# Kernel tuning notes

Hardware: AMD Instinct MI355X
Metric: run time of the kernel (lower is better)

The kernel has to match this reference:

```python
import jax, jax.numpy as jnp
import numpy as np
from jax import lax

B, N, S = 16, 8192, 512
BASE_K = 16
MS_K = (8, 16, 24)


def _fps(xyz, npoint):
    # farthest point sampling; xyz [B,N,3] -> indices [B,npoint]
    b, n, _ = xyz.shape
    def body(carry, _):
        dists, far = carry
        c = jnp.take_along_axis(xyz, far[:, None, None], axis=1)  # [B,1,3]
        d = jnp.sum((xyz - c) ** 2, -1)
        dists = jnp.minimum(dists, d)
        return (dists, jnp.argmax(dists, -1).astype(jnp.int32)), far
    init = (jnp.full((b, n), 1e10, xyz.dtype), jnp.zeros((b,), jnp.int32))
    _, idx = lax.scan(body, init, None, length=npoint)
    return idx.swapaxes(0, 1)  # [B,npoint]


def _sqdist(a, b):
    # a [B,S,3], b [B,N,3] -> squared distances [B,S,N] (same topk order as cdist)
    return (jnp.sum(a * a, -1)[:, :, None] + jnp.sum(b * b, -1)[:, None, :]
            - 2.0 * jnp.einsum('bsc,bnc->bsn', a, b))


def _gather(pts, idx):
    # pts [B,N,C], idx [B,S,K] -> [B,S,K,C]
    b = pts.shape[0]
    return pts[jnp.arange(b)[:, None, None], idx]


def setup_inputs():
    key = jax.random.key(0)
    ks = jax.random.split(key, 6)
    s = 0.05
    return {
        'l0_xyz': jax.random.normal(ks[0], (B, 3, N), jnp.float32),
        'l0_points': jax.random.normal(ks[1], (B, 3, N), jnp.float32),
        'sa_W1': jax.random.normal(ks[2], (64, 6), jnp.float32) * s,
        'sa_b1': jnp.zeros((64,), jnp.float32),
        'sa_W2': jax.random.normal(ks[3], (128, 64), jnp.float32) * s,
        'sa_b2': jnp.zeros((128,), jnp.float32),
        'ms_W1': jax.random.normal(ks[4], (3, 64, 3), jnp.float32) * s,
        'ms_b1': jnp.zeros((3, 64), jnp.float32),
        'ms_W2': jax.random.normal(ks[5], (3, 128, 64), jnp.float32) * s,
        'ms_b2': jnp.zeros((3, 128), jnp.float32),
    }


def reference(l0_xyz, l0_points, sa_W1, sa_b1, sa_W2, sa_b2, ms_W1, ms_b1, ms_W2, ms_b2):
    xyz = l0_xyz.swapaxes(1, 2)     # [B,N,3]
    pts = l0_points.swapaxes(1, 2)  # [B,N,3]
    # --- PointNet_SA_Module_KNN: FPS + KNN grouping + shared MLP + max-pool ---
    fps_idx = _fps(lax.stop_gradient(xyz), S)                         # [B,S]
    new_xyz = jnp.take_along_axis(xyz, fps_idx[:, :, None], axis=1)  # [B,S,3]
    d = _sqdist(lax.stop_gradient(new_xyz), lax.stop_gradient(xyz))  # [B,S,N]
    _, knn_idx = lax.top_k(-d, BASE_K)                                # [B,S,K]
    g_xyz = _gather(xyz, knn_idx) - new_xyz[:, :, None]               # [B,S,K,3]
    g_pts = _gather(pts, knn_idx)                                     # [B,S,K,3]
    feat = jnp.concatenate([g_xyz, g_pts], -1)                        # [B,S,K,6]
    h = jax.nn.relu(jnp.einsum('bskc,oc->bsko', feat, sa_W1) + sa_b1)
    h = jnp.einsum('bsko,po->bskp', h, sa_W2) + sa_b2
    base_feat = jnp.max(h, axis=2)                                    # [B,S,128]
    keypoints = new_xyz.swapaxes(1, 2)                                # [B,3,S]
    # --- multi-scale: no_grad cdist, per-scale topk + rel-coord MLP + max-pool ---
    dist = _sqdist(lax.stop_gradient(new_xyz), lax.stop_gradient(xyz))  # [B,S,N]
    feats = [base_feat.swapaxes(1, 2)]                                  # [B,128,S]
    for i, k in enumerate(MS_K):
        k_eff = min(k, N)
        _, idx = lax.top_k(-dist, k_eff)                                # [B,S,k]
        rel = _gather(xyz, idx) - new_xyz[:, :, None]                   # [B,S,k,3]
        h = jax.nn.relu(jnp.einsum('bskc,oc->bsko', rel, ms_W1[i]) + ms_b1[i])
        h = jnp.einsum('bsko,po->bskp', h, ms_W2[i]) + ms_b2[i]
        feats.append(jnp.max(h, axis=2).swapaxes(1, 2))                 # [B,128,S]
    return keypoints, jnp.concatenate(feats, axis=1)                    # [B,3,S],[B,512,S]
```

## Files before the change

kernel.cpp:

```cpp
#include <hip/hip_runtime.h>

#define BB 16
#define NN 8192
#define SS 512
#define N3 (3 * NN)
#define KD 14

typedef unsigned short u16;
typedef unsigned int u32;
typedef unsigned long long u64;
typedef float v2f __attribute__((ext_vector_type(2)));

__device__ __forceinline__ v2f pk_add(v2f a, v2f b) {
  v2f r;
  asm("v_pk_add_f32 %0, %1, %2" : "=v"(r) : "v"(a), "v"(b));
  return r;
}
__device__ __forceinline__ v2f pk_mul(v2f a, v2f b) {
  v2f r;
  asm("v_pk_mul_f32 %0, %1, %2" : "=v"(r) : "v"(a), "v"(b));
  return r;
}

template <int CTRL>
__device__ __forceinline__ u64 dpp_maxk(u64 k) {
  u32 lo = (u32)k, hi = (u32)(k >> 32);
  u32 slo = (u32)__builtin_amdgcn_update_dpp(0, (int)lo, CTRL, 0xf, 0xf, false);
  u32 shi = (u32)__builtin_amdgcn_update_dpp(0, (int)hi, CTRL, 0xf, 0xf, false);
  u64 s = ((u64)shi << 32) | (u64)slo;
  return (s > k) ? s : k;
}
__device__ __forceinline__ u64 maxk(u64 a, u64 b) { return (a > b) ? a : b; }

__global__ __attribute__((amdgpu_flat_work_group_size(512, 512),
                          amdgpu_waves_per_eu(2, 2)))
void k_fps(const float* __restrict__ xyz, float* __restrict__ out_kp) {
  __shared__ float sxyz[NN * 3];
  __shared__ int sIdx[SS];
  __shared__ u64 rkey[2][8];
  int b = blockIdx.x, t = threadIdx.x;
  const float* base = xyz + b * N3;
  v2f px[8], py[8], pz[8], dm[8];
#pragma unroll
  for (int j = 0; j < 8; ++j) {
    int n0 = j * 1024 + t, n1 = n0 + 512;
    px[j] = v2f{base[n0], base[n1]};
    py[j] = v2f{base[NN + n0], base[NN + n1]};
    pz[j] = v2f{base[2 * NN + n0], base[2 * NN + n1]};
    dm[j] = v2f{1e10f, 1e10f};
    sxyz[n0 * 3 + 0] = px[j].x;
    sxyz[n0 * 3 + 1] = py[j].x;
    sxyz[n0 * 3 + 2] = pz[j].x;
    sxyz[n1 * 3 + 0] = px[j].y;
    sxyz[n1 * 3 + 1] = py[j].y;
    sxyz[n1 * 3 + 2] = pz[j].y;
  }
#pragma unroll
  for (int j = 0; j < 8; ++j) {
    asm volatile("" : "+v"(px[j]), "+v"(py[j]), "+v"(pz[j]));
  }
  float cx = base[0], cy = base[NN], cz = base[2 * NN];
  int far = 0;
  int lane = t & 63, w = t >> 6;
  u32 tb = (u32)(NN - t);
  for (int it = 0; it < SS; ++it) {
    if (t == 0) sIdx[it] = far;
    v2f ncx = v2f{-cx, -cx}, ncy = v2f{-cy, -cy}, ncz = v2f{-cz, -cz};
    float vmax = 0.0f;
#pragma unroll
    for (int j = 0; j < 8; ++j) {
      v2f dx = pk_add(px[j], ncx);
      v2f dy = pk_add(py[j], ncy);
      v2f dz = pk_add(pz[j], ncz);
      v2f xx = pk_mul(dx, dx);
      v2f yy = pk_mul(dy, dy);
      v2f s = pk_add(xx, yy);
      v2f zz = pk_mul(dz, dz);
      v2f d = pk_add(s, zz);
      float a0 = fminf(dm[j].x, d.x);
      float a1 = fminf(dm[j].y, d.y);
      dm[j].x = a0;
      dm[j].y = a1;
      vmax = fmaxf(vmax, fmaxf(a0, a1));
    }
    u32 cand = 0;
#pragma unroll
    for (int j = 7; j >= 0; --j) {
      u32 v1 = tb - (u32)(j * 1024 + 512);
      u32 v0 = tb - (u32)(j * 1024);
      cand = (dm[j].y == vmax) ? v1 : cand;
      cand = (dm[j].x == vmax) ? v0 : cand;
    }
    u64 key = ((u64)__float_as_uint(vmax) << 32) | cand;
    key = dpp_maxk<0x111>(key);
    key = dpp_maxk<0x112>(key);
    key = dpp_maxk<0x114>(key);
    key = dpp_maxk<0x118>(key);
    key = dpp_maxk<0x142>(key);
    key = dpp_maxk<0x143>(key);
    int pb = it & 1;
    if (lane == 63) rkey[pb][w] = key;
    __syncthreads();
    u64 k0 = rkey[pb][0], k1 = rkey[pb][1];
    u64 k2 = rkey[pb][2], k3 = rkey[pb][3];
    u64 k4 = rkey[pb][4], k5 = rkey[pb][5];
    u64 k6 = rkey[pb][6], k7 = rkey[pb][7];
    u64 kg = maxk(maxk(maxk(k0, k1), maxk(k2, k3)),
                  maxk(maxk(k4, k5), maxk(k6, k7)));
    far = NN - (int)(u32)(kg & 0xffffffffu);
    cx = sxyz[far * 3 + 0];
    cy = sxyz[far * 3 + 1];
    cz = sxyz[far * 3 + 2];
  }
  __syncthreads();
  for (int i = t; i < SS; i += 512) {
    int id = sIdx[i];
    out_kp[b * 1536 + i] = base[id];
    out_kp[b * 1536 + SS + i] = base[NN + id];
    out_kp[b * 1536 + 2 * SS + i] = base[2 * NN + id];
  }
}

__global__ __launch_bounds__(256) void k_knn(const float* __restrict__ xyz,
                                             const float* __restrict__ kp,
                                             u16* __restrict__ knn) {
  int t = threadIdx.x;
  int row = blockIdx.x * 4 + (t >> 6);
  int lane = t & 63;
  int b = row >> 9, s = row & (SS - 1);
  const float* base = xyz + b * N3;
  float ax = kp[b * 1536 + s];
  float ay = kp[b * 1536 + SS + s];
  float az = kp[b * 1536 + 2 * SS + s];
  float aw = __fadd_rn(__fadd_rn(__fmul_rn(ax, ax), __fmul_rn(ay, ay)), __fmul_rn(az, az));
  u64 arr[KD];
#pragma unroll
  for (int i = 0; i < KD; ++i) arr[i] = ~0ull;
  for (int c = 0; c < 128; ++c) {
    int n = c * 64 + lane;
    float qx = base[n], qy = base[NN + n], qz = base[2 * NN + n];
    float qw = __fadd_rn(__fadd_rn(__fmul_rn(qx, qx), __fmul_rn(qy, qy)), __fmul_rn(qz, qz));
    float dot = __fadd_rn(__fadd_rn(__fmul_rn(ax, qx), __fmul_rn(ay, qy)), __fmul_rn(az, qz));
    float d = __fsub_rn(__fadd_rn(aw, qw), __fmul_rn(2.0f, dot));
    u32 ub = __float_as_uint(d);
    ub ^= (ub & 0x80000000u) ? 0xFFFFFFFFu : 0x80000000u;
    u64 key = ((u64)ub << 32) | (u32)n;
    if (key < arr[KD - 1]) {
#pragma unroll
      for (int i = KD - 1; i >= 1; --i) {
        u64 am = arr[i - 1];
        arr[i] = (am > key) ? am : ((arr[i] > key) ? key : arr[i]);
      }
      if (arr[0] > key) arr[0] = key;
    }
  }
  u64 mine = 0;
  for (int it = 0; it < 24; ++it) {
    u64 m = arr[0];
#pragma unroll
    for (int off = 1; off < 64; off <<= 1) {
      u64 o = __shfl_xor(m, off, 64);
      m = (o < m) ? o : m;
    }
    if (lane == it) mine = m;
    if (arr[0] == m) {
#pragma unroll
      for (int i = 0; i < KD - 1; ++i) arr[i] = arr[i + 1];
      arr[KD - 1] = ~0ull;
    }
  }
  if (lane < 24) knn[row * 24 + lane] = (u16)(mine & 0xFFFFu);
}

__global__ __launch_bounds__(256) void k_base(
    const float* __restrict__ xyz, const float* __restrict__ pts,
    const float* __restrict__ kp, const u16* __restrict__ knn,
    const float* __restrict__ W1, const float* __restrict__ b1,
    const float* __restrict__ W2, const float* __restrict__ b2,
    float* __restrict__ out) {
  __shared__ float sW1T[6 * 64];
  __shared__ float sb1[64];
  __shared__ float sfeat[4][16 * 6];
  __shared__ float sh1[4][16 * 64];
  int t = threadIdx.x, lane = t & 63, w = t >> 6;
  int b = blockIdx.x >> 6, s0 = (blockIdx.x & 63) * 8;
  for (int i = t; i < 384; i += 256) {
    int o = i / 6, c = i - o * 6;
    sW1T[c * 64 + o] = W1[i];
  }
  if (t < 64) sb1[t] = b1[t];
  float wgtA[64], wgtB[64];
#pragma unroll
  for (int j = 0; j < 64; ++j) {
    wgtA[j] = W2[lane * 64 + j];
    wgtB[j] = W2[(lane + 64) * 64 + j];
  }
  float b2A = b2[lane], b2B = b2[lane + 64];
  __syncthreads();
  for (int g = 0; g < 2; ++g) {
    for (int i = t; i < 384; i += 256) {
      int rr = i / 96, rem = i - rr * 96, k = rem / 6, c = rem - k * 6;
      int s = s0 + g * 4 + rr, row = b * SS + s;
      int id = knn[row * 24 + k];
      float val;
      if (c < 3) {
        val = __fsub_rn(xyz[b * N3 + c * NN + id], kp[b * 1536 + c * SS + s]);
      } else {
        val = pts[b * N3 + (c - 3) * NN + id];
      }
      sfeat[rr][k * 6 + c] = val;
    }
    __syncthreads();
#pragma unroll
    for (int m = 0; m < 16; ++m) {
      int u = m * 256 + t;
      int rr = u >> 10, rem = u & 1023, k = rem >> 6, o = rem & 63;
      float acc = sb1[o];
#pragma unroll
      for (int c = 0; c < 6; ++c) acc = fmaf(sfeat[rr][k * 6 + c], sW1T[c * 64 + o], acc);
      sh1[rr][k * 64 + o] = fmaxf(acc, 0.f);
    }
    __syncthreads();
    float bestA = -1e30f, bestB = -1e30f;
#pragma unroll
    for (int k = 0; k < 16; ++k) {
      const float4* h4 = (const float4*)&sh1[w][k * 64];
      float a0 = 0.f, a1 = 0.f;
#pragma unroll
      for (int j = 0; j < 16; ++j) {
        float4 hv = h4[j];
        a0 = fmaf(hv.x, wgtA[4 * j], a0);
        a0 = fmaf(hv.y, wgtA[4 * j + 1], a0);
        a0 = fmaf(hv.z, wgtA[4 * j + 2], a0);
        a0 = fmaf(hv.w, wgtA[4 * j + 3], a0);
        a1 = fmaf(hv.x, wgtB[4 * j], a1);
        a1 = fmaf(hv.y, wgtB[4 * j + 1], a1);
        a1 = fmaf(hv.z, wgtB[4 * j + 2], a1);
        a1 = fmaf(hv.w, wgtB[4 * j + 3], a1);
      }
      bestA = fmaxf(bestA, a0);
      bestB = fmaxf(bestB, a1);
    }
    int s = s0 + g * 4 + w;
    out[24576 + b * 262144 + lane * 512 + s] = bestA + b2A;
    out[24576 + b * 262144 + (lane + 64) * 512 + s] = bestB + b2B;
    __syncthreads();
  }
}

__global__ __launch_bounds__(256) void k_ms(
    const float* __restrict__ xyz, const float* __restrict__ kp,
    const u16* __restrict__ knn, const float* __restrict__ msW1,
    const float* __restrict__ msb1, const float* __restrict__ msW2,
    const float* __restrict__ msb2, float* __restrict__ out) {
  int scale = blockIdx.y;
  int kk = 8 * (scale + 1);
  __shared__ float sW1T[3 * 64];
  __shared__ float sb1[64];
  __shared__ float sfeat[4][24 * 3];
  __shared__ float sh1[4][24 * 64];
  int t = threadIdx.x, lane = t & 63, w = t >> 6;
  int b = blockIdx.x >> 6, s0 = (blockIdx.x & 63) * 8;
  const float* W1s = msW1 + scale * 192;
  for (int i = t; i < 192; i += 256) {
    int o = i / 3, c = i - o * 3;
    sW1T[c * 64 + o] = W1s[i];
  }
  if (t < 64) sb1[t] = msb1[scale * 64 + t];
  float wgtA[64], wgtB[64];
#pragma unroll
  for (int j = 0; j < 64; ++j) {
    wgtA[j] = msW2[scale * 8192 + lane * 64 + j];
    wgtB[j] = msW2[scale * 8192 + (lane + 64) * 64 + j];
  }
  float b2A = msb2[scale * 128 + lane], b2B = msb2[scale * 128 + lane + 64];
  __syncthreads();
  int co = 128 * (scale + 1);
  for (int g = 0; g < 2; ++g) {
    int nfeat = 4 * kk * 3;
    for (int i = t; i < nfeat; i += 256) {
      int kk3 = kk * 3;
      int rr = i / kk3, rem = i - rr * kk3, k = rem / 3, c = rem - k * 3;
      int s = s0 + g * 4 + rr, row = b * SS + s;
      int id = knn[row * 24 + k];
      sfeat[rr][k * 3 + c] = __fsub_rn(xyz[b * N3 + c * NN + id], kp[b * 1536 + c * SS + s]);
    }
    __syncthreads();
    for (int rr = 0; rr < 4; ++rr) {
      for (int u = t; u < kk * 64; u += 256) {
        int k = u >> 6, o = u & 63;
        float acc = sb1[o];
        acc = fmaf(sfeat[rr][k * 3 + 0], sW1T[o], acc);
        acc = fmaf(sfeat[rr][k * 3 + 1], sW1T[64 + o], acc);
        acc = fmaf(sfeat[rr][k * 3 + 2], sW1T[128 + o], acc);
        sh1[rr][k * 64 + o] = fmaxf(acc, 0.f);
      }
    }
    __syncthreads();
    float bestA = -1e30f, bestB = -1e30f;
    for (int k = 0; k < kk; ++k) {
      const float4* h4 = (const float4*)&sh1[w][k * 64];
      float a0 = 0.f, a1 = 0.f;
#pragma unroll
      for (int j = 0; j < 16; ++j) {
        float4 hv = h4[j];
        a0 = fmaf(hv.x, wgtA[4 * j], a0);
        a0 = fmaf(hv.y, wgtA[4 * j + 1], a0);
        a0 = fmaf(hv.z, wgtA[4 * j + 2], a0);
        a0 = fmaf(hv.w, wgtA[4 * j + 3], a0);
        a1 = fmaf(hv.x, wgtB[4 * j], a1);
        a1 = fmaf(hv.y, wgtB[4 * j + 1], a1);
        a1 = fmaf(hv.z, wgtB[4 * j + 2], a1);
        a1 = fmaf(hv.w, wgtB[4 * j + 3], a1);
      }
      bestA = fmaxf(bestA, a0);
      bestB = fmaxf(bestB, a1);
    }
    int s = s0 + g * 4 + w;
    out[24576 + b * 262144 + (co + lane) * 512 + s] = bestA + b2A;
    out[24576 + b * 262144 + (co + lane + 64) * 512 + s] = bestB + b2B;
    __syncthreads();
  }
}

extern "C" void kernel_launch(void* const* d_in, const int* in_sizes, int n_in,
                              void* d_out, int out_size, void* d_ws, size_t ws_size,
                              hipStream_t stream) {
  const float* xyz = (const float*)d_in[0];
  const float* pts = (const float*)d_in[1];
  const float* sa_W1 = (const float*)d_in[2];
  const float* sa_b1 = (const float*)d_in[3];
  const float* sa_W2 = (const float*)d_in[4];
  const float* sa_b2 = (const float*)d_in[5];
  const float* ms_W1 = (const float*)d_in[6];
  const float* ms_b1 = (const float*)d_in[7];
  const float* ms_W2 = (const float*)d_in[8];
  const float* ms_b2 = (const float*)d_in[9];
  float* out = (float*)d_out;
  const float* kp = (const float*)d_out;

  u16* knn = (u16*)d_ws;

  k_fps<<<BB, 512, 0, stream>>>(xyz, out);
  k_knn<<<(BB * SS) / 4, 256, 0, stream>>>(xyz, kp, knn);
  k_base<<<BB * 64, 256, 0, stream>>>(xyz, pts, kp, knn, sa_W1, sa_b1, sa_W2, sa_b2, out);
  k_ms<<<dim3(BB * 64, 3), 256, 0, stream>>>(xyz, kp, knn, ms_W1, ms_b1, ms_W2, ms_b2, out);
}
```

Baseline: 1.005 ms.

## Pack xyz/pts into float4 with precomputed norms, merge MLP kernels, simplify insertion

Adds a prep kernel that converts planar xyz and pts into AoS float4 arrays, with the squared norm stored in w. KNN and grouping then use single vector loads and skip recomputing the norm. The base and multi-scale MLP kernels are merged into one launch with a 4-wide y grid, and the feature gather now gives each thread a whole point instead of one scalar. The KNN sorted-insert is rewritten to compute all comparisons first, to shorten the dependency chain. This costs an extra kernel, workspace memory, and a fallback path that is chosen by workspace size.

```diff
diff --git a/kernel.cpp b/kernel.cpp
--- a/kernel.cpp
+++ b/kernel.cpp
@@ -31,6 +31,20 @@
   return (s > k) ? s : k;
 }
 __device__ __forceinline__ u64 maxk(u64 a, u64 b) { return (a > b) ? a : b; }
+
+__global__ __launch_bounds__(256) void k_prep(const float* __restrict__ xyz,
+                                              const float* __restrict__ pts,
+                                              float4* __restrict__ xyz4,
+                                              float4* __restrict__ pts4) {
+  int i = blockIdx.x * 256 + threadIdx.x;
+  int b = i >> 13, n = i & (NN - 1);
+  const float* xb = xyz + b * N3;
+  float x = xb[n], y = xb[NN + n], z = xb[2 * NN + n];
+  float w = __fadd_rn(__fadd_rn(__fmul_rn(x, x), __fmul_rn(y, y)), __fmul_rn(z, z));
+  xyz4[i] = make_float4(x, y, z, w);
+  const float* pb = pts + b * N3;
+  pts4[i] = make_float4(pb[n], pb[NN + n], pb[2 * NN + n], 0.f);
+}
 
 __global__ __attribute__((amdgpu_flat_work_group_size(512, 512),
                           amdgpu_waves_per_eu(2, 2)))
@@ -121,7 +135,9 @@
   }
 }
 
+template <int USE4>
 __global__ __launch_bounds__(256) void k_knn(const float* __restrict__ xyz,
+                                             const float4* __restrict__ xyz4,
                                              const float* __restrict__ kp,
                                              u16* __restrict__ knn) {
   int t = threadIdx.x;
@@ -129,6 +145,7 @@
   int lane = t & 63;
   int b = row >> 9, s = row & (SS - 1);
   const float* base = xyz + b * N3;
+  const float4* base4 = xyz4 + (b << 13);
   float ax = kp[b * 1536 + s];
   float ay = kp[b * 1536 + SS + s];
   float az = kp[b * 1536 + 2 * SS + s];
@@ -138,20 +155,27 @@
   for (int i = 0; i < KD; ++i) arr[i] = ~0ull;
   for (int c = 0; c < 128; ++c) {
     int n = c * 64 + lane;
-    float qx = base[n], qy = base[NN + n], qz = base[2 * NN + n];
-    float qw = __fadd_rn(__fadd_rn(__fmul_rn(qx, qx), __fmul_rn(qy, qy)), __fmul_rn(qz, qz));
+    float qx, qy, qz, qw;
+    if constexpr (USE4) {
+      float4 q = base4[n];
+      qx = q.x; qy = q.y; qz = q.z; qw = q.w;
+    } else {
+      qx = base[n]; qy = base[NN + n]; qz = base[2 * NN + n];
+      qw = __fadd_rn(__fadd_rn(__fmul_rn(qx, qx), __fmul_rn(qy, qy)), __fmul_rn(qz, qz));
+    }
     float dot = __fadd_rn(__fadd_rn(__fmul_rn(ax, qx), __fmul_rn(ay, qy)), __fmul_rn(az, qz));
     float d = __fsub_rn(__fadd_rn(aw, qw), __fmul_rn(2.0f, dot));
     u32 ub = __float_as_uint(d);
     ub ^= (ub & 0x80000000u) ? 0xFFFFFFFFu : 0x80000000u;
     u64 key = ((u64)ub << 32) | (u32)n;
     if (key < arr[KD - 1]) {
-#pragma unroll
-      for (int i = KD - 1; i >= 1; --i) {
-        u64 am = arr[i - 1];
-        arr[i] = (am > key) ? am : ((arr[i] > key) ? key : arr[i]);
-      }
-      if (arr[0] > key) arr[0] = key;
+      bool cg[KD];
+#pragma unroll
+      for (int i = 0; i < KD; ++i) cg[i] = arr[i] > key;
+#pragma unroll
+      for (int i = KD - 1; i >= 1; --i)
+        arr[i] = cg[i - 1] ? arr[i - 1] : (cg[i] ? key : arr[i]);
+      arr[0] = cg[0] ? key : arr[0];
     }
   }
   u64 mine = 0;
@@ -172,154 +196,185 @@
   if (lane < 24) knn[row * 24 + lane] = (u16)(mine & 0xFFFFu);
 }
 
-__global__ __launch_bounds__(256) void k_base(
+template <int USE4>
+__global__ __launch_bounds__(256) void k_mlp(
     const float* __restrict__ xyz, const float* __restrict__ pts,
+    const float4* __restrict__ xyz4, const float4* __restrict__ pts4,
     const float* __restrict__ kp, const u16* __restrict__ knn,
     const float* __restrict__ W1, const float* __restrict__ b1,
     const float* __restrict__ W2, const float* __restrict__ b2,
+    const float* __restrict__ msW1, const float* __restrict__ msb1,
+    const float* __restrict__ msW2, const float* __restrict__ msb2,
     float* __restrict__ out) {
-  __shared__ float sW1T[6 * 64];
-  __shared__ float sb1[64];
-  __shared__ float sfeat[4][16 * 6];
-  __shared__ float sh1[4][16 * 64];
+  __shared__ float smem[6688];
   int t = threadIdx.x, lane = t & 63, w = t >> 6;
   int b = blockIdx.x >> 6, s0 = (blockIdx.x & 63) * 8;
-  for (int i = t; i < 384; i += 256) {
-    int o = i / 6, c = i - o * 6;
-    sW1T[c * 64 + o] = W1[i];
-  }
-  if (t < 64) sb1[t] = b1[t];
-  float wgtA[64], wgtB[64];
-#pragma unroll
-  for (int j = 0; j < 64; ++j) {
-    wgtA[j] = W2[lane * 64 + j];
-    wgtB[j] = W2[(lane + 64) * 64 + j];
-  }
-  float b2A = b2[lane], b2B = b2[lane + 64];
-  __syncthreads();
-  for (int g = 0; g < 2; ++g) {
+  if (blockIdx.y == 0) {
+    float* sW1T = smem;
+    float* sb1 = smem + 384;
+    float* sfeat = smem + 448;
+    float* sh1 = smem + 832;
     for (int i = t; i < 384; i += 256) {
-      int rr = i / 96, rem = i - rr * 96, k = rem / 6, c = rem - k * 6;
-      int s = s0 + g * 4 + rr, row = b * SS + s;
-      int id = knn[row * 24 + k];
-      float val;
-      if (c < 3) {
-        val = __fsub_rn(xyz[b * N3 + c * NN + id], kp[b * 1536 + c * SS + s]);
-      } else {
-        val = pts[b * N3 + (c - 3) * NN + id];
-      }
-      sfeat[rr][k * 6 + c] = val;
-    }
+      int o = i / 6, c = i - o * 6;
+      sW1T[c * 64 + o] = W1[i];
+    }
+    if (t < 64) sb1[t] = b1[t];
+    float wgtA[64], wgtB[64];
+#pragma unroll
+    for (int j = 0; j < 64; ++j) {
+      wgtA[j] = W2[lane * 64 + j];
+      wgtB[j] = W2[(lane + 64) * 64 + j];
+    }
+    float b2A = b2[lane], b2B = b2[lane + 64];
     __syncthreads();
-#pragma unroll
-    for (int m = 0; m < 16; ++m) {
-      int u = m * 256 + t;
-      int rr = u >> 10, rem = u & 1023, k = rem >> 6, o = rem & 63;
-      float acc = sb1[o];
-#pragma unroll
-      for (int c = 0; c < 6; ++c) acc = fmaf(sfeat[rr][k * 6 + c], sW1T[c * 64 + o], acc);
-      sh1[rr][k * 64 + o] = fmaxf(acc, 0.f);
-    }
+    for (int g = 0; g < 2; ++g) {
+      if (t < 128) {
+        int p = t >> 1, h = t & 1;
+        int rr = p >> 4, k = p & 15;
+        int s = s0 + g * 4 + rr, row = b * SS + s;
+        int id = knn[row * 24 + k];
+        float* f = &sfeat[rr * 96 + k * 6];
+        if (h == 0) {
+          float qx, qy, qz;
+          if constexpr (USE4) {
+            float4 q = xyz4[(b << 13) + id];
+            qx = q.x; qy = q.y; qz = q.z;
+          } else {
+            qx = xyz[b * N3 + id];
+            qy = xyz[b * N3 + NN + id];
+            qz = xyz[b * N3 + 2 * NN + id];
+          }
+          f[0] = __fsub_rn(qx, kp[b * 1536 + s]);
+          f[1] = __fsub_rn(qy, kp[b * 1536 + SS + s]);
+          f[2] = __fsub_rn(qz, kp[b * 1536 + 2 * SS + s]);
+        } else {
+          float px_, py_, pz_;
+          if constexpr (USE4) {
+            float4 q = pts4[(b << 13) + id];
+            px_ = q.x; py_ = q.y; pz_ = q.z;
+          } else {
+            px_ = pts[b * N3 + id];
+            py_ = pts[b * N3 + NN + id];
+            pz_ = pts[b * N3 + 2 * NN + id];
+          }
+          f[3] = px_;
+          f[4] = py_;
+          f[5] = pz_;
+        }
+      }
+      __syncthreads();
+#pragma unroll
+      for (int m = 0; m < 16; ++m) {
+        int u = m * 256 + t;
+        int rr = u >> 10, rem = u & 1023, k = rem >> 6, o = rem & 63;
+        float acc = sb1[o];
+#pragma unroll
+        for (int c = 0; c < 6; ++c) acc = fmaf(sfeat[rr * 96 + k * 6 + c], sW1T[c * 64 + o], acc);
+        sh1[rr * 1024 + k * 64 + o] = fmaxf(acc, 0.f);
+      }
+      __syncthreads();
+      float bestA = -1e30f, bestB = -1e30f;
+#pragma unroll
+      for (int k = 0; k < 16; ++k) {
+        const float4* h4 = (const float4*)&sh1[w * 1024 + k * 64];
+        float a0 = 0.f, a1 = 0.f;
+#pragma unroll
+        for (int j = 0; j < 16; ++j) {
+          float4 hv = h4[j];
+          a0 = fmaf(hv.x, wgtA[4 * j], a0);
+          a0 = fmaf(hv.y, wgtA[4 * j + 1], a0);
+          a0 = fmaf(hv.z, wgtA[4 * j + 2], a0);
+          a0 = fmaf(hv.w, wgtA[4 * j + 3], a0);
+          a1 = fmaf(hv.x, wgtB[4 * j], a1);
+          a1 = fmaf(hv.y, wgtB[4 * j + 1], a1);
+          a1 = fmaf(hv.z, wgtB[4 * j + 2], a1);
+          a1 = fmaf(hv.w, wgtB[4 * j + 3], a1);
+        }
+        bestA = fmaxf(bestA, a0);
+        bestB = fmaxf(bestB, a1);
+      }
+      int s = s0 + g * 4 + w;
+      out[24576 + b * 262144 + lane * 512 + s] = bestA + b2A;
+      out[24576 + b * 262144 + (lane + 64) * 512 + s] = bestB + b2B;
+      __syncthreads();
+    }
+  } else {
+    int scale = blockIdx.y - 1;
+    int kk = 8 * (scale + 1);
+    float* sW1T = smem;
+    float* sb1 = smem + 192;
+    float* sfeat = smem + 256;
+    float* sh1 = smem + 544;
+    const float* W1s = msW1 + scale * 192;
+    for (int i = t; i < 192; i += 256) {
+      int o = i / 3, c = i - o * 3;
+      sW1T[c * 64 + o] = W1s[i];
+    }
+    if (t < 64) sb1[t] = msb1[scale * 64 + t];
+    float wgtA[64], wgtB[64];
+#pragma unroll
+    for (int j = 0; j < 64; ++j) {
+      wgtA[j] = msW2[scale * 8192 + lane * 64 + j];
+      wgtB[j] = msW2[scale * 8192 + (lane + 64) * 64 + j];
+    }
+    float b2A = msb2[scale * 128 + lane], b2B = msb2[scale * 128 + lane + 64];
     __syncthreads();
-    float bestA = -1e30f, bestB = -1e30f;
-#pragma unroll
-    for (int k = 0; k < 16; ++k) {
-      const float4* h4 = (const float4*)&sh1[w][k * 64];
-      float a0 = 0.f, a1 = 0.f;
-#pragma unroll
-      for (int j = 0; j < 16; ++j) {
-        float4 hv = h4[j];
-        a0 = fmaf(hv.x, wgtA[4 * j], a0);
-        a0 = fmaf(hv.y, wgtA[4 * j + 1], a0);
-        a0 = fmaf(hv.z, wgtA[4 * j + 2], a0);
-        a0 = fmaf(hv.w, wgtA[4 * j + 3], a0);
-        a1 = fmaf(hv.x, wgtB[4 * j], a1);
-        a1 = fmaf(hv.y, wgtB[4 * j + 1], a1);
-        a1 = fmaf(hv.z, wgtB[4 * j + 2], a1);
-        a1 = fmaf(hv.w, wgtB[4 * j + 3], a1);
-      }
-      bestA = fmaxf(bestA, a0);
-      bestB = fmaxf(bestB, a1);
-    }
-    int s = s0 + g * 4 + w;
-    out[24576 + b * 262144 + lane * 512 + s] = bestA + b2A;
-    out[24576 + b * 262144 + (lane + 64) * 512 + s] = bestB + b2B;
-    __syncthreads();
-  }
-}
-
-__global__ __launch_bounds__(256) void k_ms(
-    const float* __restrict__ xyz, const float* __restrict__ kp,
-    const u16* __restrict__ knn, const float* __restrict__ msW1,
-    const float* __restrict__ msb1, const float* __restrict__ msW2,
-    const float* __restrict__ msb2, float* __restrict__ out) {
-  int scale = blockIdx.y;
-  int kk = 8 * (scale + 1);
-  __shared__ float sW1T[3 * 64];
-  __shared__ float sb1[64];
-  __shared__ float sfeat[4][24 * 3];
-  __shared__ float sh1[4][24 * 64];
-  int t = threadIdx.x, lane = t & 63, w = t >> 6;
-  int b = blockIdx.x >> 6, s0 = (blockIdx.x & 63) * 8;
-  const float* W1s = msW1 + scale * 192;
-  for (int i = t; i < 192; i += 256) {
-    int o = i / 3, c = i - o * 3;
-    sW1T[c * 64 + o] = W1s[i];
-  }
-  if (t < 64) sb1[t] = msb1[scale * 64 + t];
-  float wgtA[64], wgtB[64];
-#pragma unroll
-  for (int j = 0; j < 64; ++j) {
-    wgtA[j] = msW2[scale * 8192 + lane * 64 + j];
-    wgtB[j] = msW2[scale * 8192 + (lane + 64) * 64 + j];
-  }
-  float b2A = msb2[scale * 128 + lane], b2B = msb2[scale * 128 + lane + 64];
-  __syncthreads();
-  int co = 128 * (scale + 1);
-  for (int g = 0; g < 2; ++g) {
-    int nfeat = 4 * kk * 3;
-    for (int i = t; i < nfeat; i += 256) {
-      int kk3 = kk * 3;
-      int rr = i / kk3, rem = i - rr * kk3, k = rem / 3, c = rem - k * 3;
-      int s = s0 + g * 4 + rr, row = b * SS + s;
-      int id = knn[row * 24 + k];
-      sfeat[rr][k * 3 + c] = __fsub_rn(xyz[b * N3 + c * NN + id], kp[b * 1536 + c * SS + s]);
-    }
-    __syncthreads();
-    for (int rr = 0; rr < 4; ++rr) {
-      for (int u = t; u < kk * 64; u += 256) {
-        int k = u >> 6, o = u & 63;
-        float acc = sb1[o];
-        acc = fmaf(sfeat[rr][k * 3 + 0], sW1T[o], acc);
-        acc = fmaf(sfeat[rr][k * 3 + 1], sW1T[64 + o], acc);
-        acc = fmaf(sfeat[rr][k * 3 + 2], sW1T[128 + o], acc);
-        sh1[rr][k * 64 + o] = fmaxf(acc, 0.f);
-      }
-    }
-    __syncthreads();
-    float bestA = -1e30f, bestB = -1e30f;
-    for (int k = 0; k < kk; ++k) {
-      const float4* h4 = (const float4*)&sh1[w][k * 64];
-      float a0 = 0.f, a1 = 0.f;
-#pragma unroll
-      for (int j = 0; j < 16; ++j) {
-        float4 hv = h4[j];
-        a0 = fmaf(hv.x, wgtA[4 * j], a0);
-        a0 = fmaf(hv.y, wgtA[4 * j + 1], a0);
-        a0 = fmaf(hv.z, wgtA[4 * j + 2], a0);
-        a0 = fmaf(hv.w, wgtA[4 * j + 3], a0);
-        a1 = fmaf(hv.x, wgtB[4 * j], a1);
-        a1 = fmaf(hv.y, wgtB[4 * j + 1], a1);
-        a1 = fmaf(hv.z, wgtB[4 * j + 2], a1);
-        a1 = fmaf(hv.w, wgtB[4 * j + 3], a1);
-      }
-      bestA = fmaxf(bestA, a0);
-      bestB = fmaxf(bestB, a1);
-    }
-    int s = s0 + g * 4 + w;
-    out[24576 + b * 262144 + (co + lane) * 512 + s] = bestA + b2A;
-    out[24576 + b * 262144 + (co + lane + 64) * 512 + s] = bestB + b2B;
-    __syncthreads();
+    int co = 128 * (scale + 1);
+    for (int g = 0; g < 2; ++g) {
+      if (t < 96) {
+        int rr = t / 24, k = t - rr * 24;
+        int s = s0 + g * 4 + rr, row = b * SS + s;
+        int id = knn[row * 24 + k];
+        float qx, qy, qz;
+        if constexpr (USE4) {
+          float4 q = xyz4[(b << 13) + id];
+          qx = q.x; qy = q.y; qz = q.z;
+        } else {
+          qx = xyz[b * N3 + id];
+          qy = xyz[b * N3 + NN + id];
+          qz = xyz[b * N3 + 2 * NN + id];
+        }
+        float* f = &sfeat[rr * 72 + k * 3];
+        f[0] = __fsub_rn(qx, kp[b * 1536 + s]);
+        f[1] = __fsub_rn(qy, kp[b * 1536 + SS + s]);
+        f[2] = __fsub_rn(qz, kp[b * 1536 + 2 * SS + s]);
+      }
+      __syncthreads();
+      for (int rr = 0; rr < 4; ++rr) {
+        for (int u = t; u < kk * 64; u += 256) {
+          int k = u >> 6, o = u & 63;
+          float acc = sb1[o];
+          acc = fmaf(sfeat[rr * 72 + k * 3 + 0], sW1T[o], acc);
+          acc = fmaf(sfeat[rr * 72 + k * 3 + 1], sW1T[64 + o], acc);
+          acc = fmaf(sfeat[rr * 72 + k * 3 + 2], sW1T[128 + o], acc);
+          sh1[rr * 1536 + k * 64 + o] = fmaxf(acc, 0.f);
+        }
+      }
+      __syncthreads();
+      float bestA = -1e30f, bestB = -1e30f;
+      for (int k = 0; k < kk; ++k) {
+        const float4* h4 = (const float4*)&sh1[w * 1536 + k * 64];
+        float a0 = 0.f, a1 = 0.f;
+#pragma unroll
+        for (int j = 0; j < 16; ++j) {
+          float4 hv = h4[j];
+          a0 = fmaf(hv.x, wgtA[4 * j], a0);
+          a0 = fmaf(hv.y, wgtA[4 * j + 1], a0);
+          a0 = fmaf(hv.z, wgtA[4 * j + 2], a0);
+          a0 = fmaf(hv.w, wgtA[4 * j + 3], a0);
+          a1 = fmaf(hv.x, wgtB[4 * j], a1);
+          a1 = fmaf(hv.y, wgtB[4 * j + 1], a1);
+          a1 = fmaf(hv.z, wgtB[4 * j + 2], a1);
+          a1 = fmaf(hv.w, wgtB[4 * j + 3], a1);
+        }
+        bestA = fmaxf(bestA, a0);
+        bestB = fmaxf(bestB, a1);
+      }
+      int s = s0 + g * 4 + w;
+      out[24576 + b * 262144 + (co + lane) * 512 + s] = bestA + b2A;
+      out[24576 + b * 262144 + (co + lane + 64) * 512 + s] = bestB + b2B;
+      __syncthreads();
+    }
   }
 }
 
@@ -340,9 +395,22 @@
   const float* kp = (const float*)d_out;
 
   u16* knn = (u16*)d_ws;
-
+  float4* xyz4 = (float4*)((char*)d_ws + 393216);
+  float4* pts4 = xyz4 + BB * NN;
+  const size_t need4 = 393216 + (size_t)2 * BB * NN * sizeof(float4);
+  const bool use4 = ws_size >= need4;
+
+  if (use4) k_prep<<<BB * NN / 256, 256, 0, stream>>>(xyz, pts, xyz4, pts4);
   k_fps<<<BB, 512, 0, stream>>>(xyz, out);
-  k_knn<<<(BB * SS) / 4, 256, 0, stream>>>(xyz, kp, knn);
-  k_base<<<BB * 64, 256, 0, stream>>>(xyz, pts, kp, knn, sa_W1, sa_b1, sa_W2, sa_b2, out);
-  k_ms<<<dim3(BB * 64, 3), 256, 0, stream>>>(xyz, kp, knn, ms_W1, ms_b1, ms_W2, ms_b2, out);
-}
+  if (use4) {
+    k_knn<1><<<(BB * SS) / 4, 256, 0, stream>>>(xyz, xyz4, kp, knn);
+    k_mlp<1><<<dim3(BB * 64, 4), 256, 0, stream>>>(xyz, pts, xyz4, pts4, kp, knn,
+                                                   sa_W1, sa_b1, sa_W2, sa_b2,
+                                                   ms_W1, ms_b1, ms_W2, ms_b2, out);
+  } else {
+    k_knn<0><<<(BB * SS) / 4, 256, 0, stream>>>(xyz, xyz4, kp, knn);
+    k_mlp<0><<<dim3(BB * 64, 4), 256, 0, stream>>>(xyz, pts, xyz4, pts4, kp, knn,
+                                                   sa_W1, sa_b1, sa_W2, sa_b2,
+                                                   ms_W1, ms_b1, ms_W2, ms_b2, out);
+  }
+}
```

After: 967.1 us. 3.8% less time.
